# Optimization experiments

Hardware: AMD Instinct MI355X
Metric: run time of the kernel (lower is better)

Reference implementation:

```python
import jax, jax.numpy as jnp
import numpy as np

# config (matches init_kwargs)
B, H, N, D = 2, 8, 2048, 64
ALPHA = 1.0        # < 2 -> power-law kernel branch
D_INT = 4.0        # d_intrinsic
BW = 1.0           # bandwidth
A = 0.5            # dual-sided degree-normalization exponent
R = 1.0            # sphere_radius
MASK_VAL = 10000.0
EPS = 1e-7


def setup_inputs() -> dict:
    key = jax.random.key(0)
    k1, k2, k3, k4 = jax.random.split(key, 4)
    Q = jax.random.normal(k1, (B, H, N, D), dtype=jnp.float32)
    K = jax.random.normal(k2, (B, H, N, D), dtype=jnp.float32)
    V = jax.random.normal(k3, (B, H, N, D), dtype=jnp.float32)
    mask = jax.random.randint(k4, (B, N), 0, 2).astype(jnp.int32)
    return {"Q": Q, "K": K, "V": V, "mask": mask}


def reference(Q, K, V, mask) -> jnp.ndarray:
    # geodesic distance on the sphere: acos(clamp(QK^T)) * radius  [B,H,N,N]
    qk = jnp.einsum('bhnd,bhmd->bhnm', Q, K)
    g_dist = jnp.arccos(jnp.clip(qk, -1.0 + EPS, 1.0 - EPS)) * R
    # key-side padding mask: [B,N] -> [B,1,1,N]
    g_dist = jnp.where(mask[:, None, None, :] == 0, MASK_VAL, g_dist)
    # power-law kernel (alpha < 2 branch)
    attn_score = (1.0 + g_dist / jnp.sqrt(BW)) ** (-D_INT - ALPHA)
    # dual-sided degree normalization (a != 0 branch)
    n_r = jnp.sum(attn_score, axis=-1)   # row degrees [B,H,N]
    n_c = jnp.sum(attn_score, axis=-2)   # col degrees [B,H,N]
    k_tilde = (n_r ** (-A))[..., :, None] * attn_score * (n_c ** (-A))[..., None, :]
    # F.normalize(p=1, dim=3)
    attn = k_tilde / jnp.maximum(jnp.sum(jnp.abs(k_tilde), axis=-1, keepdims=True), 1e-12)
    # dropout p=0.0 -> identity
    return jnp.einsum('bhnm,bhmd->bhnd', attn, V)
```

## Files before the change

### kernel.cpp

```cpp
#include <hip/hip_runtime.h>
#include <hip/hip_bf16.h>
#include <math.h>

#define B_ 2
#define H_ 8
#define N_ 2048
#define D_ 64
#define BH_ 16
#define NT_ (N_/64)
#define LS 72
#define LSW (LS/2)

typedef __attribute__((ext_vector_type(8))) short short8;
typedef __attribute__((ext_vector_type(4))) float float4v;
typedef __attribute__((ext_vector_type(2))) float float2v;

__device__ __forceinline__ float2v splat2(float s){ float2v v; v.x=s; v.y=s; return v; }

__device__ __forceinline__ unsigned packbf2(float a, float b){
  __hip_bfloat162 h = __float22bfloat162_rn(make_float2(a, b));
  return *(unsigned*)&h;
}
__device__ __forceinline__ void split2(float a, float b, unsigned& hi, unsigned& lo){
  hi = packbf2(a, b);
  float ha = __uint_as_float(hi << 16);
  float hb = __uint_as_float(hi & 0xFFFF0000u);
  lo = packbf2(a - ha, b - hb);
}
__device__ __forceinline__ void load_split8(const float* p, short8& hi8, short8& lo8){
  float4v v0 = *(const float4v*)p;
  float4v v1 = *(const float4v*)(p + 4);
  unsigned h0,h1,h2,h3,l0,l1,l2,l3;
  split2(v0.x, v0.y, h0, l0);
  split2(v0.z, v0.w, h1, l1);
  split2(v1.x, v1.y, h2, l2);
  split2(v1.z, v1.w, h3, l3);
  unsigned ph[4] = {h0,h1,h2,h3};
  unsigned pl[4] = {l0,l1,l2,l3};
  hi8 = *(short8*)ph;
  lo8 = *(short8*)pl;
}

__device__ __forceinline__ float2v score2(float2v qk){
  float2v ax;
  ax.x = fminf(fabsf(qk.x), 1.0f - 1e-7f);
  ax.y = fminf(fabsf(qk.y), 1.0f - 1e-7f);
  float2v p = __builtin_elementwise_fma(
                __builtin_elementwise_fma(
                  __builtin_elementwise_fma(splat2(-0.0187293f), ax, splat2(0.0742610f)),
                  ax, splat2(-0.2121144f)),
                ax, splat2(1.5707288f));
  float2v u = __builtin_elementwise_fma(ax, splat2(-1.0f), splat2(1.0f));
  float2v t;
  t.x = __builtin_amdgcn_sqrtf(u.x);
  t.y = __builtin_amdgcn_sqrtf(u.y);
  float2v t2 = t * p;
  float2v gn = __builtin_elementwise_fma(t2, splat2(-1.0f), splat2(3.14159265358979f));
  float2v g;
  g.x = (qk.x >= 0.0f) ? t2.x : gn.x;
  g.y = (qk.y >= 0.0f) ? t2.y : gn.y;
  float2v w1 = g + splat2(1.0f);
  float2v w2 = w1 * w1;
  float2v w4 = w2 * w2;
  float2v w5 = w4 * w1;
  float2v r;
  r.x = __builtin_amdgcn_rcpf(w5.x);
  r.y = __builtin_amdgcn_rcpf(w5.y);
  return r;
}

__device__ __forceinline__ float score_fn_m(float qk, float masked){
  float ax = fminf(fabsf(qk), 1.0f - 1e-7f);
  float t  = __builtin_amdgcn_sqrtf(1.0f - ax);
  float p  = __builtin_fmaf(__builtin_fmaf(__builtin_fmaf(-0.0187293f, ax, 0.0742610f),
                                           ax, -0.2121144f), ax, 1.5707288f);
  float t2 = t * p;
  float g  = (qk >= 0.0f) ? t2 : (3.14159265358979f - t2);
  g = (masked != 0.0f) ? 10000.0f : g;
  float w1 = 1.0f + g;
  float w2 = w1*w1;
  float w4 = w2*w2;
  return __builtin_amdgcn_rcpf(w4*w1);
}

__global__ __launch_bounds__(256) void k0_split(
    const float* __restrict__ Q, const float* __restrict__ K,
    unsigned short* __restrict__ Qh, unsigned short* __restrict__ Ql,
    unsigned short* __restrict__ Kh, unsigned short* __restrict__ Kl)
{
  size_t i = (size_t)blockIdx.x*256 + threadIdx.x;
  const size_t tot = (size_t)BH_*N_*D_/8;
  const float* src; unsigned short *dh, *dl;
  if (i < tot){ src = Q; dh = Qh; dl = Ql; }
  else        { src = K; dh = Kh; dl = Kl; i -= tot; }
  short8 hi, lo;
  load_split8(src + i*8, hi, lo);
  *(short8*)&dh[i*8] = hi;
  *(short8*)&dl[i*8] = lo;
}

template<bool PRE>
__global__ __launch_bounds__(256) void k1_score(
    const float* __restrict__ Qf, const float* __restrict__ Kf,
    const unsigned short* __restrict__ Qh, const unsigned short* __restrict__ Ql,
    const unsigned short* __restrict__ Kh, const unsigned short* __restrict__ Kl,
    float* __restrict__ ncw, unsigned short* __restrict__ S)
{
  __shared__ float red[64*4];
  const int kt = blockIdx.x, bh = blockIdx.y, rz = blockIdx.z;
  const int nz = gridDim.z;
  const int tid = threadIdx.x;
  const int wv = tid>>6, lane = tid&63, quad = lane>>4, l15 = lane&15;

  short8 khi[4][2], klo[4][2];
  if constexpr (PRE){
    #pragma unroll
    for (int s=0;s<4;++s){
      const size_t r = (size_t)(bh*N_ + kt*64 + s*16 + l15)*D_ + quad*8;
      khi[s][0] = *(const short8*)&Kh[r];
      khi[s][1] = *(const short8*)&Kh[r+32];
      klo[s][0] = *(const short8*)&Kl[r];
      klo[s][1] = *(const short8*)&Kl[r+32];
    }
  } else {
    #pragma unroll
    for (int s=0;s<4;++s){
      const float* kp = Kf + (size_t)(bh*N_ + kt*64 + s*16 + l15)*D_ + quad*8;
      load_split8(kp,      khi[s][0], klo[s][0]);
      load_split8(kp + 32, khi[s][1], klo[s][1]);
    }
  }

  float2v cs2[4][2];
  #pragma unroll
  for (int s=0;s<4;++s){ cs2[s][0] = splat2(0.f); cs2[s][1] = splat2(0.f); }

  const int iters = NT_/nz;
  const int rt0 = rz*iters;

  const size_t qoff0 = (size_t)(bh*N_ + rt0*64 + wv*16 + l15)*D_ + quad*8;
  const unsigned lconst = (unsigned)(((quad>>1)<<7) + (l15<<3) + ((quad&1)<<2));
  unsigned short* Sp = S + ((((size_t)(bh*NT_ + kt)*NT_ + rt0)*4 + wv)<<10) + lconst;

  short8 qh0,qh1,ql0,ql1;
  if constexpr (PRE){
    const unsigned short* qp = Qh + qoff0;
    const unsigned short* lp = Ql + qoff0;
    qh0 = *(const short8*)qp;      qh1 = *(const short8*)(qp+32);
    ql0 = *(const short8*)lp;      ql1 = *(const short8*)(lp+32);
  } else {
    const float* qp = Qf + qoff0;
    load_split8(qp,      qh0, ql0);
    load_split8(qp + 32, qh1, ql1);
  }

  for (int rti=0; rti<iters; ++rti){
    short8 nh0,nh1,nl0,nl1;
    const size_t qoffn = qoff0 + (size_t)(rti + ((rti+1<iters) ? 1 : 0))*4096;
    if constexpr (PRE){
      const unsigned short* qp = Qh + qoffn;
      const unsigned short* lp = Ql + qoffn;
      nh0 = *(const short8*)qp;    nh1 = *(const short8*)(qp+32);
      nl0 = *(const short8*)lp;    nl1 = *(const short8*)(lp+32);
    } else {
      const float* qp = Qf + qoffn;
      load_split8(qp,      nh0, nl0);
      load_split8(qp + 32, nh1, nl1);
    }

    #pragma unroll
    for (int s=0;s<4;++s){
      float4v c = {0.f,0.f,0.f,0.f};
      c = __builtin_amdgcn_mfma_f32_16x16x32_bf16(khi[s][0], qh0, c, 0,0,0);
      c = __builtin_amdgcn_mfma_f32_16x16x32_bf16(khi[s][0], ql0, c, 0,0,0);
      c = __builtin_amdgcn_mfma_f32_16x16x32_bf16(klo[s][0], qh0, c, 0,0,0);
      c = __builtin_amdgcn_mfma_f32_16x16x32_bf16(khi[s][1], qh1, c, 0,0,0);
      c = __builtin_amdgcn_mfma_f32_16x16x32_bf16(khi[s][1], ql1, c, 0,0,0);
      c = __builtin_amdgcn_mfma_f32_16x16x32_bf16(klo[s][1], qh1, c, 0,0,0);
      float2v c01; c01.x = c[0]; c01.y = c[1];
      float2v c23; c23.x = c[2]; c23.y = c[3];
      float2v s01 = score2(c01);
      float2v s23 = score2(c23);
      cs2[s][0] += s01;
      cs2[s][1] += s23;
      uint2 pk;
      pk.x = packbf2(s01.x, s01.y);
      pk.y = packbf2(s23.x, s23.y);
      *(uint2*)(Sp + (s<<8)) = pk;
    }
    Sp += 4096;
    qh0=nh0; qh1=nh1; ql0=nl0; ql1=nl1;
  }

  float cs[4][4];
  #pragma unroll
  for (int s=0;s<4;++s){
    cs[s][0]=cs2[s][0].x; cs[s][1]=cs2[s][0].y;
    cs[s][2]=cs2[s][1].x; cs[s][3]=cs2[s][1].y;
  }

  #pragma unroll
  for (int s=0;s<4;++s)
    #pragma unroll
    for (int i=0;i<4;++i){
      float v2 = cs[s][i];
      v2 += __shfl_xor(v2, 1);
      v2 += __shfl_xor(v2, 2);
      v2 += __shfl_xor(v2, 4);
      v2 += __shfl_xor(v2, 8);
      cs[s][i] = v2;
    }
  if (l15 == 0){
    #pragma unroll
    for (int s=0;s<4;++s)
      #pragma unroll
      for (int i=0;i<4;++i)
        red[(s*16 + quad*4 + i)*4 + wv] = cs[s][i];
  }
  __syncthreads();
  if (tid < 64){
    float t = red[tid*4+0] + red[tid*4+1] + red[tid*4+2] + red[tid*4+3];
    atomicAdd(&ncw[bh*N_ + kt*64 + tid], t);
  }
}

__global__ __launch_bounds__(256) void k2_pack(
    const float* __restrict__ V, const float* __restrict__ nc,
    const int* __restrict__ mask, unsigned short* __restrict__ Vw)
{
  __shared__ float T[64*65];
  __shared__ float wrow[64];
  const int mt = blockIdx.x, bh = blockIdx.y;
  const int tid = threadIdx.x;
  const float* Vg = V + (size_t)bh*N_*D_;
  const float* ncg = nc + (size_t)bh*N_;
  unsigned short* Fb = Vw + ((size_t)(bh*NT_ + mt)*10)*512;

  {
    int m = tid >> 2;
    int d0 = (tid & 3) * 16;
    int gm = mt*64 + m;
    float wm = (mask[(bh>>3)*N_ + gm] == 0) ? 0.0f
             : (1.0f / sqrtf(fmaxf(ncg[gm], 1e-30f)));
    if (d0 == 0) wrow[m] = wm;
    #pragma unroll
    for (int j=0;j<4;++j){
      float4v v = *(const float4v*)(Vg + (size_t)gm*D_ + d0 + j*4);
      T[(d0+j*4+0)*65 + m] = v.x*wm;
      T[(d0+j*4+1)*65 + m] = v.y*wm;
      T[(d0+j*4+2)*65 + m] = v.z*wm;
      T[(d0+j*4+3)*65 + m] = v.w*wm;
    }
  }
  __syncthreads();

  for (int idx = tid; idx < 640; idx += 256){
    int f = idx >> 6, lane = idx & 63;
    int quad = lane >> 4, l15 = lane & 15;
    int s2 = f >> 1, cc = f & 1;
    int m0 = cc*32 + quad*8;
    unsigned pk[4];
    if (s2 < 4){
      int d = s2*16 + l15;
      #pragma unroll
      for (int j=0;j<4;++j)
        pk[j] = packbf2(T[d*65 + m0 + 2*j], T[d*65 + m0 + 2*j + 1]);
    } else if (l15 == 0){
      #pragma unroll
      for (int j=0;j<4;++j)
        pk[j] = packbf2(wrow[m0 + 2*j], wrow[m0 + 2*j + 1]);
    } else {
      pk[0]=pk[1]=pk[2]=pk[3]=0u;
    }
    *(short8*)(Fb + ((size_t)f*64 + lane)*8) = *(short8*)pk;
  }
}

__global__ __launch_bounds__(1024) void k3_lds(
    const unsigned short* __restrict__ S, const unsigned short* __restrict__ Vw,
    float* __restrict__ out)
{
  __shared__ unsigned short Vs[2*2*10*512];

  const int rtp = blockIdx.x, bh = blockIdx.y;
  const int tid = threadIdx.x;
  const int wvid = tid >> 6;
  const int g    = wvid >> 3;
  const int slot = wvid & 7;
  const int lane = tid & 63, quad = lane >> 4, l15 = lane & 15;

  const int row = rtp*128 + slot*16 + l15;
  const int rt  = rtp*2 + (slot>>2);

  const size_t sb0 = ((((size_t)bh*NT_ + g*16)*NT_ + rt)*4 + (size_t)(slot&3))*1024
                   + (size_t)quad*128 + (size_t)l15*8;

  float4v acc[4];
  #pragma unroll
  for (int i=0;i<4;++i) acc[i] = (float4v){0.f,0.f,0.f,0.f};
  float4v c5 = {0.f,0.f,0.f,0.f};

  for (int c = tid; c < 1280; c += 1024){
    const int gg = (c >= 640) ? 1 : 0;
    const int rem = c - gg*640;
    const int f = rem >> 6, ln = rem & 63;
    const int kt = gg*16;
    *(short8*)&Vs[(((0*2 + gg)*10 + f) << 9) + ln*8] =
      *(const short8*)&Vw[(((size_t)(bh*NT_ + kt)*10 + f) << 9) + ln*8];
  }
  short8 npf0, npf1;
  npf0 = *(const short8*)&S[sb0];
  npf1 = *(const short8*)&S[sb0 + 512];
  __syncthreads();

  for (int it = 0; it < 16; ++it){
    const int cur = it & 1, nxt = cur ^ 1;
    short8 pf0 = npf0, pf1 = npf1;
    if (it < 15){
      const size_t sb = sb0 + (size_t)(it+1)*131072;
      npf0 = *(const short8*)&S[sb];
      npf1 = *(const short8*)&S[sb + 512];
      for (int c = tid; c < 1280; c += 1024){
        const int gg = (c >= 640) ? 1 : 0;
        const int rem = c - gg*640;
        const int f = rem >> 6, ln = rem & 63;
        const int kt2 = gg*16 + it + 1;
        *(short8*)&Vs[(((nxt*2 + gg)*10 + f) << 9) + ln*8] =
          *(const short8*)&Vw[(((size_t)(bh*NT_ + kt2)*10 + f) << 9) + ln*8];
      }
    }
    const unsigned short* Fl = &Vs[((cur*2 + g)*10) << 9] + (size_t)lane*8;
    short8 va[10];
    #pragma unroll
    for (int f=0; f<10; ++f)
      va[f] = *(const short8*)(Fl + ((size_t)f << 9));

    #pragma unroll
    for (int s2=0;s2<4;++s2){
      acc[s2] = __builtin_amdgcn_mfma_f32_16x16x32_bf16(va[s2*2+0], pf0, acc[s2], 0,0,0);
      acc[s2] = __builtin_amdgcn_mfma_f32_16x16x32_bf16(va[s2*2+1], pf1, acc[s2], 0,0,0);
    }
    c5 = __builtin_amdgcn_mfma_f32_16x16x32_bf16(va[8], pf0, c5, 0,0,0);
    c5 = __builtin_amdgcn_mfma_f32_16x16x32_bf16(va[9], pf1, c5, 0,0,0);

    __syncthreads();
  }

  float* Red = (float*)Vs;
  if (g == 1){
    float* Rr = Red + (size_t)(slot*16 + l15)*68;
    #pragma unroll
    for (int s2=0;s2<4;++s2)
      #pragma unroll
      for (int i=0;i<4;++i)
        Rr[s2*16 + quad*4 + i] = acc[s2][i];
    if (quad == 0) Rr[64] = c5[0];
  }
  __syncthreads();
  if (g == 0){
    const float* Rr = Red + (size_t)(slot*16 + l15)*68;
    #pragma unroll
    for (int s2=0;s2<4;++s2)
      #pragma unroll
      for (int i=0;i<4;++i)
        acc[s2][i] += Rr[s2*16 + quad*4 + i];
    float rs = __shfl(c5[0], l15) + Rr[64];
    float inv = 1.0f / fmaxf(rs, 1e-12f);

    float* Og = out + (size_t)bh*N_*D_ + (size_t)row*D_;
    #pragma unroll
    for (int s2=0;s2<4;++s2)
      #pragma unroll
      for (int i=0;i<4;++i)
        Og[s2*16 + quad*4 + i] = acc[s2][i] * inv;
  }
}

__global__ __launch_bounds__(256) void k1_fallback(
    const float* __restrict__ Q, const float* __restrict__ K,
    const int* __restrict__ mask, float* __restrict__ ncw)
{
  __shared__ float msk[64];
  __shared__ float red[64*4];
  const int kt = blockIdx.x, bh = blockIdx.y;
  const int tid = threadIdx.x;
  const int wv = tid>>6, lane = tid&63, quad = lane>>4, l15 = lane&15;

  const float* Qg = Q + (size_t)bh*N_*D_;
  const float* Kg = K + (size_t)bh*N_*D_;

  short8 khi[4][2], klo[4][2];
  #pragma unroll
  for (int s=0;s<4;++s){
    const float* kp = Kg + (size_t)(kt*64 + s*16 + l15)*D_ + quad*8;
    load_split8(kp,      khi[s][0], klo[s][0]);
    load_split8(kp + 32, khi[s][1], klo[s][1]);
  }
  if (tid < 64)
    msk[tid] = (mask[(bh>>3)*N_ + kt*64 + tid] == 0) ? 1.f : 0.f;
  __syncthreads();

  float cs[4][4];
  #pragma unroll
  for (int s=0;s<4;++s)
    #pragma unroll
    for (int i=0;i<4;++i) cs[s][i] = 0.f;

  for (int rt=0; rt<NT_; ++rt){
    const float* qp = Qg + (size_t)(rt*64 + wv*16 + l15)*D_ + quad*8;
    short8 bhi[2], blo[2];
    load_split8(qp,      bhi[0], blo[0]);
    load_split8(qp + 32, bhi[1], blo[1]);

    #pragma unroll
    for (int s=0;s<4;++s){
      float4v c = {0.f,0.f,0.f,0.f};
      #pragma unroll
      for (int cc=0; cc<2; ++cc){
        c = __builtin_amdgcn_mfma_f32_16x16x32_bf16(khi[s][cc], bhi[cc], c, 0,0,0);
        c = __builtin_amdgcn_mfma_f32_16x16x32_bf16(khi[s][cc], blo[cc], c, 0,0,0);
        c = __builtin_amdgcn_mfma_f32_16x16x32_bf16(klo[s][cc], bhi[cc], c, 0,0,0);
      }
      int kl = s*16 + quad*4;
      cs[s][0] += score_fn_m(c[0], msk[kl+0]);
      cs[s][1] += score_fn_m(c[1], msk[kl+1]);
      cs[s][2] += score_fn_m(c[2], msk[kl+2]);
      cs[s][3] += score_fn_m(c[3], msk[kl+3]);
    }
  }

  #pragma unroll
  for (int s=0;s<4;++s)
    #pragma unroll
    for (int i=0;i<4;++i){
      float v2 = cs[s][i];
      v2 += __shfl_xor(v2, 1);
      v2 += __shfl_xor(v2, 2);
      v2 += __shfl_xor(v2, 4);
      v2 += __shfl_xor(v2, 8);
      cs[s][i] = v2;
    }
  if (l15 == 0){
    #pragma unroll
    for (int s=0;s<4;++s)
      #pragma unroll
      for (int i=0;i<4;++i)
        red[(s*16 + quad*4 + i)*4 + wv] = cs[s][i];
  }
  __syncthreads();
  if (tid < 64){
    float t = red[tid*4+0] + red[tid*4+1] + red[tid*4+2] + red[tid*4+3];
    ncw[bh*N_ + kt*64 + tid] = 1.0f / sqrtf(t);
  }
}

__global__ __launch_bounds__(256) void spop_pass2(
    const float* __restrict__ Q, const float* __restrict__ K,
    const float* __restrict__ V, const int* __restrict__ mask,
    const float* __restrict__ w, float* __restrict__ out)
{
  __shared__ unsigned short Khi[64*LS], Klo[64*LS];
  __shared__ unsigned short Vt[64*LS];
  __shared__ unsigned short Ps[64*LS];
  __shared__ float msk[64], wms[64];

  const int rt = blockIdx.x, bh = blockIdx.y, b = bh>>3;
  const int tid = threadIdx.x;
  const int wv = tid>>6, lane = tid&63, quad = lane>>4, l15 = lane&15;

  const float* Qg = Q + (size_t)bh*N_*D_;
  const float* Kg = K + (size_t)bh*N_*D_;
  const float* Vg = V + (size_t)bh*N_*D_;

  short8 qhi[2], qlo[2];
  {
    const float* qp = Qg + (size_t)(rt*64 + wv*16 + l15)*D_ + quad*8;
    load_split8(qp,      qhi[0], qlo[0]);
    load_split8(qp + 32, qhi[1], qlo[1]);
  }

  float4v acc[4];
  #pragma unroll
  for (int i=0;i<4;++i) acc[i] = (float4v){0.f,0.f,0.f,0.f};
  float rs = 0.f;

  for (int kt=0; kt<NT_; ++kt){
    __syncthreads();
    #pragma unroll
    for (int it=0; it<4; ++it){
      int idx = tid + it*256;
      int r = idx>>4, d4 = (idx&15)<<2;
      const float4v v = *(const float4v*)(Kg + (size_t)(kt*64 + r)*D_ + d4);
      unsigned h0,l0,h1,l1;
      split2(v.x, v.y, h0, l0);
      split2(v.z, v.w, h1, l1);
      unsigned* KhiW = (unsigned*)Khi; unsigned* KloW = (unsigned*)Klo;
      int base = r*LSW + (d4>>1);
      KhiW[base] = h0; KhiW[base+1] = h1;
      KloW[base] = l0; KloW[base+1] = l1;
    }
    #pragma unroll
    for (int it=0; it<2; ++it){
      int u = tid + it*256;
      int kp = u & 31;
      int d4 = (u>>5)<<2;
      const float* vp = Vg + (size_t)(kt*64 + kp*2)*D_ + d4;
      float4v a0 = *(const float4v*)vp;
      float4v a1 = *(const float4v*)(vp + D_);
      unsigned* VtW = (unsigned*)Vt;
      VtW[(d4+0)*LSW + kp] = packbf2(a0.x, a1.x);
      VtW[(d4+1)*LSW + kp] = packbf2(a0.y, a1.y);
      VtW[(d4+2)*LSW + kp] = packbf2(a0.z, a1.z);
      VtW[(d4+3)*LSW + kp] = packbf2(a0.w, a1.w);
    }
    if (tid < 64){
      int gk = kt*64 + tid;
      msk[tid] = (mask[b*N_ + gk] == 0) ? 1.f : 0.f;
      wms[tid] = w[bh*N_ + gk];
    }
    __syncthreads();

    #pragma unroll
    for (int s=0;s<4;++s){
      float4v c = {0.f,0.f,0.f,0.f};
      #pragma unroll
      for (int cc=0; cc<2; ++cc){
        const short8 ahi = *(const short8*)&Khi[(s*16+l15)*LS + cc*32 + quad*8];
        const short8 alo = *(const short8*)&Klo[(s*16+l15)*LS + cc*32 + quad*8];
        c = __builtin_amdgcn_mfma_f32_16x16x32_bf16(ahi, qhi[cc], c, 0,0,0);
        c = __builtin_amdgcn_mfma_f32_16x16x32_bf16(ahi, qlo[cc], c, 0,0,0);
        c = __builtin_amdgcn_mfma_f32_16x16x32_bf16(alo, qhi[cc], c, 0,0,0);
      }
      int kl = s*16 + quad*4;
      float sc0 = score_fn_m(c[0], msk[kl+0]) * wms[kl+0];
      float sc1 = score_fn_m(c[1], msk[kl+1]) * wms[kl+1];
      float sc2 = score_fn_m(c[2], msk[kl+2]) * wms[kl+2];
      float sc3 = score_fn_m(c[3], msk[kl+3]) * wms[kl+3];
      rs += (sc0 + sc1) + (sc2 + sc3);
      unsigned* PsW = (unsigned*)Ps;
      int pb = (wv*16 + l15)*LSW + (kl>>1);
      PsW[pb]   = packbf2(sc0, sc1);
      PsW[pb+1] = packbf2(sc2, sc3);
    }

    short8 pf[2];
    pf[0] = *(const short8*)&Ps[(wv*16+l15)*LS +  0 + quad*8];
    pf[1] = *(const short8*)&Ps[(wv*16+l15)*LS + 32 + quad*8];
    #pragma unroll
    for (int s2=0;s2<4;++s2){
      #pragma unroll
      for (int cc=0; cc<2; ++cc){
        const short8 av = *(const short8*)&Vt[(s2*16+l15)*LS + cc*32 + quad*8];
        acc[s2] = __builtin_amdgcn_mfma_f32_16x16x32_bf16(av, pf[cc], acc[s2], 0,0,0);
      }
    }
  }

  rs += __shfl_xor(rs, 16);
  rs += __shfl_xor(rs, 32);
  float inv = 1.0f / fmaxf(rs, 1e-12f);

  float* Og = out + (size_t)bh*N_*D_ + (size_t)(rt*64 + wv*16 + l15)*D_;
  #pragma unroll
  for (int s2=0;s2<4;++s2)
    #pragma unroll
    for (int i=0;i<4;++i)
      Og[s2*16 + quad*4 + i] = acc[s2][i] * inv;
}

extern "C" void kernel_launch(void* const* d_in, const int* in_sizes, int n_in,
                              void* d_out, int out_size, void* d_ws, size_t ws_size,
                              hipStream_t stream) {
  (void)in_sizes; (void)n_in; (void)out_size;
  const float* Q   = (const float*)d_in[0];
  const float* K   = (const float*)d_in[1];
  const float* V   = (const float*)d_in[2];
  const int*  mask = (const int*)d_in[3];
  float* out = (float*)d_out;

  const size_t nc_bytes = (size_t)BH_*N_*sizeof(float);
  const size_t vw_off   = 131072;
  const size_t vw_bytes = (size_t)BH_*NT_*10*512*2;
  const size_t qk_off   = vw_off + vw_bytes;
  const size_t qk_one   = (size_t)BH_*N_*D_;
  const size_t qk_bytes = 4*qk_one*2;
  const size_t S_bytes  = (size_t)2*BH_*N_*N_;
  const size_t need_A   = qk_off + qk_bytes + S_bytes;
  const size_t need_B   = qk_off + S_bytes;

  if (ws_size >= need_A){
    float* nc = (float*)d_ws;
    unsigned short* Vw = (unsigned short*)((char*)d_ws + vw_off);
    unsigned short* Qh = (unsigned short*)((char*)d_ws + qk_off);
    unsigned short* Ql = Qh + qk_one;
    unsigned short* Kh = Ql + qk_one;
    unsigned short* Kl = Kh + qk_one;
    unsigned short* S  = (unsigned short*)((char*)d_ws + qk_off + qk_bytes);
    hipMemsetAsync(nc, 0, nc_bytes, stream);
    k0_split<<<dim3(2048), 256, 0, stream>>>(Q, K, Qh, Ql, Kh, Kl);
    k1_score<true><<<dim3(NT_, BH_, 4), 256, 0, stream>>>(
        nullptr, nullptr, Qh, Ql, Kh, Kl, nc, S);
    k2_pack<<<dim3(NT_, BH_), 256, 0, stream>>>(V, nc, mask, Vw);
    k3_lds<<<dim3(N_/128, BH_), 1024, 0, stream>>>(S, Vw, out);
  } else if (ws_size >= need_B){
    float* nc = (float*)d_ws;
    unsigned short* Vw = (unsigned short*)((char*)d_ws + vw_off);
    unsigned short* S  = (unsigned short*)((char*)d_ws + qk_off);
    hipMemsetAsync(nc, 0, nc_bytes, stream);
    k1_score<false><<<dim3(NT_, BH_, 4), 256, 0, stream>>>(
        Q, K, nullptr, nullptr, nullptr, nullptr, nc, S);
    k2_pack<<<dim3(NT_, BH_), 256, 0, stream>>>(V, nc, mask, Vw);
    k3_lds<<<dim3(N_/128, BH_), 1024, 0, stream>>>(S, Vw, out);
  } else {
    float* w = (float*)d_ws;
    k1_fallback<<<dim3(NT_, BH_), 256, 0, stream>>>(Q, K, mask, w);
    spop_pass2<<<dim3(NT_, BH_), 256, 0, stream>>>(Q, K, V, mask, w, out);
  }
}
```

Baseline: 171.4 us.

## Give each score wave its own key tile and defer V staging stores past MFMAs

The score kernel now assigns each wave a distinct 16-key slice and loops over all query row tiles with one MFMA chain per iteration. This drops the shared-memory reduction and barrier in favour of per-wave atomics, and adds a launch-bounds occupancy hint. The PV kernel loads the next V tile into registers before the MFMAs and writes it to LDS afterwards, so global latency overlaps compute. The trade-off is four times more Q reloads per block, more atomics, and no Q prefetch across iterations.

```diff
diff --git a/kernel.cpp b/kernel.cpp
--- a/kernel.cpp
+++ b/kernel.cpp
@@ -100,127 +100,87 @@
 }
 
 template<bool PRE>
-__global__ __launch_bounds__(256) void k1_score(
+__global__ __launch_bounds__(256, 8) void k1_score(
     const float* __restrict__ Qf, const float* __restrict__ Kf,
     const unsigned short* __restrict__ Qh, const unsigned short* __restrict__ Ql,
     const unsigned short* __restrict__ Kh, const unsigned short* __restrict__ Kl,
     float* __restrict__ ncw, unsigned short* __restrict__ S)
 {
-  __shared__ float red[64*4];
   const int kt = blockIdx.x, bh = blockIdx.y, rz = blockIdx.z;
   const int nz = gridDim.z;
   const int tid = threadIdx.x;
   const int wv = tid>>6, lane = tid&63, quad = lane>>4, l15 = lane&15;
 
-  short8 khi[4][2], klo[4][2];
-  if constexpr (PRE){
-    #pragma unroll
-    for (int s=0;s<4;++s){
-      const size_t r = (size_t)(bh*N_ + kt*64 + s*16 + l15)*D_ + quad*8;
-      khi[s][0] = *(const short8*)&Kh[r];
-      khi[s][1] = *(const short8*)&Kh[r+32];
-      klo[s][0] = *(const short8*)&Kl[r];
-      klo[s][1] = *(const short8*)&Kl[r+32];
-    }
-  } else {
-    #pragma unroll
-    for (int s=0;s<4;++s){
-      const float* kp = Kf + (size_t)(bh*N_ + kt*64 + s*16 + l15)*D_ + quad*8;
-      load_split8(kp,      khi[s][0], klo[s][0]);
-      load_split8(kp + 32, khi[s][1], klo[s][1]);
-    }
-  }
-
-  float2v cs2[4][2];
-  #pragma unroll
-  for (int s=0;s<4;++s){ cs2[s][0] = splat2(0.f); cs2[s][1] = splat2(0.f); }
-
-  const int iters = NT_/nz;
-  const int rt0 = rz*iters;
-
-  const size_t qoff0 = (size_t)(bh*N_ + rt0*64 + wv*16 + l15)*D_ + quad*8;
-  const unsigned lconst = (unsigned)(((quad>>1)<<7) + (l15<<3) + ((quad&1)<<2));
-  unsigned short* Sp = S + ((((size_t)(bh*NT_ + kt)*NT_ + rt0)*4 + wv)<<10) + lconst;
-
-  short8 qh0,qh1,ql0,ql1;
-  if constexpr (PRE){
-    const unsigned short* qp = Qh + qoff0;
-    const unsigned short* lp = Ql + qoff0;
-    qh0 = *(const short8*)qp;      qh1 = *(const short8*)(qp+32);
-    ql0 = *(const short8*)lp;      ql1 = *(const short8*)(lp+32);
-  } else {
-    const float* qp = Qf + qoff0;
-    load_split8(qp,      qh0, ql0);
-    load_split8(qp + 32, qh1, ql1);
-  }
-
-  for (int rti=0; rti<iters; ++rti){
-    short8 nh0,nh1,nl0,nl1;
-    const size_t qoffn = qoff0 + (size_t)(rti + ((rti+1<iters) ? 1 : 0))*4096;
+  short8 khi[2], klo[2];
+  {
+    const size_t r = (size_t)(bh*N_ + kt*64 + wv*16 + l15)*D_ + quad*8;
     if constexpr (PRE){
-      const unsigned short* qp = Qh + qoffn;
-      const unsigned short* lp = Ql + qoffn;
-      nh0 = *(const short8*)qp;    nh1 = *(const short8*)(qp+32);
-      nl0 = *(const short8*)lp;    nl1 = *(const short8*)(lp+32);
+      khi[0] = *(const short8*)&Kh[r];
+      khi[1] = *(const short8*)&Kh[r+32];
+      klo[0] = *(const short8*)&Kl[r];
+      klo[1] = *(const short8*)&Kl[r+32];
     } else {
-      const float* qp = Qf + qoffn;
-      load_split8(qp,      nh0, nl0);
-      load_split8(qp + 32, nh1, nl1);
-    }
-
-    #pragma unroll
-    for (int s=0;s<4;++s){
-      float4v c = {0.f,0.f,0.f,0.f};
-      c = __builtin_amdgcn_mfma_f32_16x16x32_bf16(khi[s][0], qh0, c, 0,0,0);
-      c = __builtin_amdgcn_mfma_f32_16x16x32_bf16(khi[s][0], ql0, c, 0,0,0);
-      c = __builtin_amdgcn_mfma_f32_16x16x32_bf16(klo[s][0], qh0, c, 0,0,0);
-      c = __builtin_amdgcn_mfma_f32_16x16x32_bf16(khi[s][1], qh1, c, 0,0,0);
-      c = __builtin_amdgcn_mfma_f32_16x16x32_bf16(khi[s][1], ql1, c, 0,0,0);
-      c = __builtin_amdgcn_mfma_f32_16x16x32_bf16(klo[s][1], qh1, c, 0,0,0);
-      float2v c01; c01.x = c[0]; c01.y = c[1];
-      float2v c23; c23.x = c[2]; c23.y = c[3];
-      float2v s01 = score2(c01);
-      float2v s23 = score2(c23);
-      cs2[s][0] += s01;
-      cs2[s][1] += s23;
-      uint2 pk;
-      pk.x = packbf2(s01.x, s01.y);
-      pk.y = packbf2(s23.x, s23.y);
-      *(uint2*)(Sp + (s<<8)) = pk;
-    }
-    Sp += 4096;
-    qh0=nh0; qh1=nh1; ql0=nl0; ql1=nl1;
-  }
-
-  float cs[4][4];
-  #pragma unroll
-  for (int s=0;s<4;++s){
-    cs[s][0]=cs2[s][0].x; cs[s][1]=cs2[s][0].y;
-    cs[s][2]=cs2[s][1].x; cs[s][3]=cs2[s][1].y;
-  }
-
-  #pragma unroll
-  for (int s=0;s<4;++s)
-    #pragma unroll
-    for (int i=0;i<4;++i){
-      float v2 = cs[s][i];
-      v2 += __shfl_xor(v2, 1);
-      v2 += __shfl_xor(v2, 2);
-      v2 += __shfl_xor(v2, 4);
-      v2 += __shfl_xor(v2, 8);
-      cs[s][i] = v2;
-    }
+      load_split8(Kf + r,      khi[0], klo[0]);
+      load_split8(Kf + r + 32, khi[1], klo[1]);
+    }
+  }
+
+  float2v cs01 = splat2(0.f), cs23 = splat2(0.f);
+
+  const int iters = (N_/16)/nz;
+  const int row0  = rz*(N_/nz);
+
+  size_t qoff = (size_t)(bh*N_ + row0 + l15)*D_ + quad*8;
+  const unsigned lconst = (unsigned)((wv<<8) + ((quad>>1)<<7) + (l15<<3) + ((quad&1)<<2));
+  unsigned short* Sp = S + (((size_t)(bh*NT_ + kt)*128 + (unsigned)(row0>>4))<<10) + lconst;
+
+  for (int j=0; j<iters; ++j){
+    short8 qh0,qh1,ql0,ql1;
+    if constexpr (PRE){
+      qh0 = *(const short8*)&Qh[qoff];  qh1 = *(const short8*)&Qh[qoff+32];
+      ql0 = *(const short8*)&Ql[qoff];  ql1 = *(const short8*)&Ql[qoff+32];
+    } else {
+      load_split8(Qf + qoff,      qh0, ql0);
+      load_split8(Qf + qoff + 32, qh1, ql1);
+    }
+
+    float4v c = {0.f,0.f,0.f,0.f};
+    c = __builtin_amdgcn_mfma_f32_16x16x32_bf16(khi[0], qh0, c, 0,0,0);
+    c = __builtin_amdgcn_mfma_f32_16x16x32_bf16(khi[0], ql0, c, 0,0,0);
+    c = __builtin_amdgcn_mfma_f32_16x16x32_bf16(klo[0], qh0, c, 0,0,0);
+    c = __builtin_amdgcn_mfma_f32_16x16x32_bf16(khi[1], qh1, c, 0,0,0);
+    c = __builtin_amdgcn_mfma_f32_16x16x32_bf16(khi[1], ql1, c, 0,0,0);
+    c = __builtin_amdgcn_mfma_f32_16x16x32_bf16(klo[1], qh1, c, 0,0,0);
+
+    float2v c01; c01.x = c[0]; c01.y = c[1];
+    float2v c23; c23.x = c[2]; c23.y = c[3];
+    float2v s01 = score2(c01);
+    float2v s23 = score2(c23);
+    cs01 += s01;
+    cs23 += s23;
+    uint2 pk;
+    pk.x = packbf2(s01.x, s01.y);
+    pk.y = packbf2(s23.x, s23.y);
+    *(uint2*)Sp = pk;
+
+    Sp += 1024;
+    qoff += (size_t)16*D_;
+  }
+
+  float cs[4] = {cs01.x, cs01.y, cs23.x, cs23.y};
+  #pragma unroll
+  for (int i=0;i<4;++i){
+    float v2 = cs[i];
+    v2 += __shfl_xor(v2, 1);
+    v2 += __shfl_xor(v2, 2);
+    v2 += __shfl_xor(v2, 4);
+    v2 += __shfl_xor(v2, 8);
+    cs[i] = v2;
+  }
   if (l15 == 0){
     #pragma unroll
-    for (int s=0;s<4;++s)
-      #pragma unroll
-      for (int i=0;i<4;++i)
-        red[(s*16 + quad*4 + i)*4 + wv] = cs[s][i];
-  }
-  __syncthreads();
-  if (tid < 64){
-    float t = red[tid*4+0] + red[tid*4+1] + red[tid*4+2] + red[tid*4+3];
-    atomicAdd(&ncw[bh*N_ + kt*64 + tid], t);
+    for (int i=0;i<4;++i)
+      atomicAdd(&ncw[bh*N_ + kt*64 + wv*16 + quad*4 + i], cs[i]);
   }
 }
 
@@ -295,40 +255,44 @@
   const size_t sb0 = ((((size_t)bh*NT_ + g*16)*NT_ + rt)*4 + (size_t)(slot&3))*1024
                    + (size_t)quad*128 + (size_t)l15*8;
 
+  const int gg0 = (tid >= 640) ? 1 : 0;
+  const int rem0 = tid - gg0*640;
+  const int f0 = rem0 >> 6, ln0 = rem0 & 63;
+  const bool has1 = (tid < 256);
+  const int rem1 = tid + 384;
+  const int f1 = rem1 >> 6, ln1 = rem1 & 63;
+  const size_t vwbh = (size_t)bh*NT_;
+
   float4v acc[4];
   #pragma unroll
   for (int i=0;i<4;++i) acc[i] = (float4v){0.f,0.f,0.f,0.f};
   float4v c5 = {0.f,0.f,0.f,0.f};
 
-  for (int c = tid; c < 1280; c += 1024){
-    const int gg = (c >= 640) ? 1 : 0;
-    const int rem = c - gg*640;
-    const int f = rem >> 6, ln = rem & 63;
-    const int kt = gg*16;
-    *(short8*)&Vs[(((0*2 + gg)*10 + f) << 9) + ln*8] =
-      *(const short8*)&Vw[(((size_t)(bh*NT_ + kt)*10 + f) << 9) + ln*8];
-  }
-  short8 npf0, npf1;
-  npf0 = *(const short8*)&S[sb0];
-  npf1 = *(const short8*)&S[sb0 + 512];
+  {
+    short8 a = *(const short8*)&Vw[(((vwbh + gg0*16)*10 + f0) << 9) + ln0*8];
+    *(short8*)&Vs[((gg0*10 + f0) << 9) + ln0*8] = a;
+    if (has1){
+      short8 b = *(const short8*)&Vw[(((vwbh + 16)*10 + f1) << 9) + ln1*8];
+      *(short8*)&Vs[((1*10 + f1) << 9) + ln1*8] = b;
+    }
+  }
+  short8 npf0 = *(const short8*)&S[sb0];
+  short8 npf1 = *(const short8*)&S[sb0 + 512];
   __syncthreads();
 
   for (int it = 0; it < 16; ++it){
     const int cur = it & 1, nxt = cur ^ 1;
     short8 pf0 = npf0, pf1 = npf1;
+    short8 vwa, vwb;
     if (it < 15){
+      vwa = *(const short8*)&Vw[(((vwbh + (size_t)(gg0*16 + it + 1))*10 + f0) << 9) + ln0*8];
+      if (has1)
+        vwb = *(const short8*)&Vw[(((vwbh + (size_t)(16 + it + 1))*10 + f1) << 9) + ln1*8];
       const size_t sb = sb0 + (size_t)(it+1)*131072;
       npf0 = *(const short8*)&S[sb];
       npf1 = *(const short8*)&S[sb + 512];
-      for (int c = tid; c < 1280; c += 1024){
-        const int gg = (c >= 640) ? 1 : 0;
-        const int rem = c - gg*640;
-        const int f = rem >> 6, ln = rem & 63;
-        const int kt2 = gg*16 + it + 1;
-        *(short8*)&Vs[(((nxt*2 + gg)*10 + f) << 9) + ln*8] =
-          *(const short8*)&Vw[(((size_t)(bh*NT_ + kt2)*10 + f) << 9) + ln*8];
-      }
-    }
+    }
+
     const unsigned short* Fl = &Vs[((cur*2 + g)*10) << 9] + (size_t)lane*8;
     short8 va[10];
     #pragma unroll
@@ -343,6 +307,11 @@
     c5 = __builtin_amdgcn_mfma_f32_16x16x32_bf16(va[8], pf0, c5, 0,0,0);
     c5 = __builtin_amdgcn_mfma_f32_16x16x32_bf16(va[9], pf1, c5, 0,0,0);
 
+    if (it < 15){
+      *(short8*)&Vs[(((nxt*2 + gg0)*10 + f0) << 9) + ln0*8] = vwa;
+      if (has1)
+        *(short8*)&Vs[(((nxt*2 + 1)*10 + f1) << 9) + ln1*8] = vwb;
+    }
     __syncthreads();
   }
 
```

Measured after the change: 231.1 us. 34.9% more time.

## Replace LDS-staged V tiles with direct global loads in final matmul kernel

Applied to the files above, without the earlier changes.

The final S·V kernel stops staging packed V fragments through double-buffered shared memory with per-iteration barriers. Each wave now loads its V fragments straight from global memory (relying on cache), and S fragments are prefetched two tiles ahead with two register sets. Blocks shrink from 1024 to 512 threads covering 64 rows instead of 128, which doubles the grid. V reuse across waves now depends on L1/L2 hits rather than explicit shared-memory sharing.

```diff
diff --git a/kernel.cpp b/kernel.cpp
--- a/kernel.cpp
+++ b/kernel.cpp
@@ -276,77 +276,79 @@
   }
 }
 
-__global__ __launch_bounds__(1024) void k3_lds(
+__global__ __launch_bounds__(512) void k3_direct(
     const unsigned short* __restrict__ S, const unsigned short* __restrict__ Vw,
     float* __restrict__ out)
 {
-  __shared__ unsigned short Vs[2*2*10*512];
-
-  const int rtp = blockIdx.x, bh = blockIdx.y;
+  __shared__ float Red[64*68];
+
+  const int rt = blockIdx.x, bh = blockIdx.y;
   const int tid = threadIdx.x;
   const int wvid = tid >> 6;
-  const int g    = wvid >> 3;
-  const int slot = wvid & 7;
+  const int g    = wvid >> 2;
+  const int slot = wvid & 3;
   const int lane = tid & 63, quad = lane >> 4, l15 = lane & 15;
-
-  const int row = rtp*128 + slot*16 + l15;
-  const int rt  = rtp*2 + (slot>>2);
-
-  const size_t sb0 = ((((size_t)bh*NT_ + g*16)*NT_ + rt)*4 + (size_t)(slot&3))*1024
+  const int row = rt*64 + slot*16 + l15;
+
+  const size_t sb0 = ((((size_t)bh*NT_ + g*16)*NT_ + rt)*4 + (size_t)slot)*1024
                    + (size_t)quad*128 + (size_t)l15*8;
+  const unsigned short* Vb = Vw + ((size_t)(bh*NT_ + g*16)*10)*512 + (size_t)lane*8;
 
   float4v acc[4];
   #pragma unroll
   for (int i=0;i<4;++i) acc[i] = (float4v){0.f,0.f,0.f,0.f};
   float4v c5 = {0.f,0.f,0.f,0.f};
 
-  for (int c = tid; c < 1280; c += 1024){
-    const int gg = (c >= 640) ? 1 : 0;
-    const int rem = c - gg*640;
-    const int f = rem >> 6, ln = rem & 63;
-    const int kt = gg*16;
-    *(short8*)&Vs[(((0*2 + gg)*10 + f) << 9) + ln*8] =
-      *(const short8*)&Vw[(((size_t)(bh*NT_ + kt)*10 + f) << 9) + ln*8];
-  }
-  short8 npf0, npf1;
-  npf0 = *(const short8*)&S[sb0];
-  npf1 = *(const short8*)&S[sb0 + 512];
-  __syncthreads();
-
-  for (int it = 0; it < 16; ++it){
-    const int cur = it & 1, nxt = cur ^ 1;
-    short8 pf0 = npf0, pf1 = npf1;
-    if (it < 15){
-      const size_t sb = sb0 + (size_t)(it+1)*131072;
-      npf0 = *(const short8*)&S[sb];
-      npf1 = *(const short8*)&S[sb + 512];
-      for (int c = tid; c < 1280; c += 1024){
-        const int gg = (c >= 640) ? 1 : 0;
-        const int rem = c - gg*640;
-        const int f = rem >> 6, ln = rem & 63;
-        const int kt2 = gg*16 + it + 1;
-        *(short8*)&Vs[(((nxt*2 + gg)*10 + f) << 9) + ln*8] =
-          *(const short8*)&Vw[(((size_t)(bh*NT_ + kt2)*10 + f) << 9) + ln*8];
+  short8 sA0 = *(const short8*)&S[sb0];
+  short8 sA1 = *(const short8*)&S[sb0 + 512];
+  short8 sB0 = *(const short8*)&S[sb0 + 131072];
+  short8 sB1 = *(const short8*)&S[sb0 + 131072 + 512];
+
+  #pragma unroll 1
+  for (int k2 = 0; k2 < 8; ++k2){
+    const int ktA = k2*2, ktB = k2*2 + 1;
+    {
+      const unsigned short* Vp = Vb + (size_t)ktA*5120;
+      short8 va[10];
+      #pragma unroll
+      for (int f=0; f<10; ++f)
+        va[f] = *(const short8*)(Vp + (size_t)f*512);
+      short8 p0 = sA0, p1 = sA1;
+      if (ktA + 2 < 16){
+        const size_t sb = sb0 + (size_t)(ktA+2)*131072;
+        sA0 = *(const short8*)&S[sb];
+        sA1 = *(const short8*)&S[sb + 512];
       }
-    }
-    const unsigned short* Fl = &Vs[((cur*2 + g)*10) << 9] + (size_t)lane*8;
-    short8 va[10];
-    #pragma unroll
-    for (int f=0; f<10; ++f)
-      va[f] = *(const short8*)(Fl + ((size_t)f << 9));
-
-    #pragma unroll
-    for (int s2=0;s2<4;++s2){
-      acc[s2] = __builtin_amdgcn_mfma_f32_16x16x32_bf16(va[s2*2+0], pf0, acc[s2], 0,0,0);
-      acc[s2] = __builtin_amdgcn_mfma_f32_16x16x32_bf16(va[s2*2+1], pf1, acc[s2], 0,0,0);
-    }
-    c5 = __builtin_amdgcn_mfma_f32_16x16x32_bf16(va[8], pf0, c5, 0,0,0);
-    c5 = __builtin_amdgcn_mfma_f32_16x16x32_bf16(va[9], pf1, c5, 0,0,0);
-
-    __syncthreads();
-  }
-
-  float* Red = (float*)Vs;
+      #pragma unroll
+      for (int s2=0;s2<4;++s2){
+        acc[s2] = __builtin_amdgcn_mfma_f32_16x16x32_bf16(va[s2*2+0], p0, acc[s2], 0,0,0);
+        acc[s2] = __builtin_amdgcn_mfma_f32_16x16x32_bf16(va[s2*2+1], p1, acc[s2], 0,0,0);
+      }
+      c5 = __builtin_amdgcn_mfma_f32_16x16x32_bf16(va[8], p0, c5, 0,0,0);
+      c5 = __builtin_amdgcn_mfma_f32_16x16x32_bf16(va[9], p1, c5, 0,0,0);
+    }
+    {
+      const unsigned short* Vp = Vb + (size_t)ktB*5120;
+      short8 va[10];
+      #pragma unroll
+      for (int f=0; f<10; ++f)
+        va[f] = *(const short8*)(Vp + (size_t)f*512);
+      short8 p0 = sB0, p1 = sB1;
+      if (ktB + 2 < 16){
+        const size_t sb = sb0 + (size_t)(ktB+2)*131072;
+        sB0 = *(const short8*)&S[sb];
+        sB1 = *(const short8*)&S[sb + 512];
+      }
+      #pragma unroll
+      for (int s2=0;s2<4;++s2){
+        acc[s2] = __builtin_amdgcn_mfma_f32_16x16x32_bf16(va[s2*2+0], p0, acc[s2], 0,0,0);
+        acc[s2] = __builtin_amdgcn_mfma_f32_16x16x32_bf16(va[s2*2+1], p1, acc[s2], 0,0,0);
+      }
+      c5 = __builtin_amdgcn_mfma_f32_16x16x32_bf16(va[8], p0, c5, 0,0,0);
+      c5 = __builtin_amdgcn_mfma_f32_16x16x32_bf16(va[9], p1, c5, 0,0,0);
+    }
+  }
+
   if (g == 1){
     float* Rr = Red + (size_t)(slot*16 + l15)*68;
     #pragma unroll
@@ -601,7 +603,7 @@
     k1_score<true><<<dim3(NT_, BH_, 4), 256, 0, stream>>>(
         nullptr, nullptr, Qh, Ql, Kh, Kl, nc, S);
     k2_pack<<<dim3(NT_, BH_), 256, 0, stream>>>(V, nc, mask, Vw);
-    k3_lds<<<dim3(N_/128, BH_), 1024, 0, stream>>>(S, Vw, out);
+    k3_direct<<<dim3(NT_, BH_), 512, 0, stream>>>(S, Vw, out);
   } else if (ws_size >= need_B){
     float* nc = (float*)d_ws;
     unsigned short* Vw = (unsigned short*)((char*)d_ws + vw_off);
@@ -610,7 +612,7 @@
     k1_score<false><<<dim3(NT_, BH_, 4), 256, 0, stream>>>(
         Q, K, nullptr, nullptr, nullptr, nullptr, nc, S);
     k2_pack<<<dim3(NT_, BH_), 256, 0, stream>>>(V, nc, mask, Vw);
-    k3_lds<<<dim3(N_/128, BH_), 1024, 0, stream>>>(S, Vw, out);
+    k3_direct<<<dim3(NT_, BH_), 512, 0, stream>>>(S, Vw, out);
   } else {
     float* w = (float*)d_ws;
     k1_fallback<<<dim3(NT_, BH_), 256, 0, stream>>>(Q, K, mask, w);
```

Measured after the change: 171.8 us. No clear change (+0.2%).

## Remap block ids so each XCD owns whole heads; register-stage V prefetch

Applied to the files above, without the earlier changes.

Launches k1, k2 and k3 as flat 1D grids and decodes block ids so that all blocks touching the same (batch, head) land on the same XCD (id & 7). This is meant to keep each head's K/Q/S/V traffic inside one XCD's L2 instead of spreading it across all eight. In k3 the next V tile is now loaded into registers before the MFMA work and written to LDS after it, rather than copied to LDS right away. The copy loop is also replaced by precomputed per-thread indices, which lets the global load latency overlap with compute at the cost of extra registers.

```diff
diff --git a/kernel.cpp b/kernel.cpp
--- a/kernel.cpp
+++ b/kernel.cpp
@@ -107,8 +107,14 @@
     float* __restrict__ ncw, unsigned short* __restrict__ S)
 {
   __shared__ float red[64*4];
-  const int kt = blockIdx.x, bh = blockIdx.y, rz = blockIdx.z;
-  const int nz = gridDim.z;
+  const int id = blockIdx.x;
+  const int xcd = id & 7;
+  const int r0 = id >> 3;
+  const int kt = r0 & 31;
+  const int grp = r0 >> 5;
+  const int flat = grp*8 + xcd;
+  const int bh = flat & 15;
+  const int rz = flat >> 4;
   const int tid = threadIdx.x;
   const int wv = tid>>6, lane = tid&63, quad = lane>>4, l15 = lane&15;
 
@@ -135,7 +141,7 @@
   #pragma unroll
   for (int s=0;s<4;++s){ cs2[s][0] = splat2(0.f); cs2[s][1] = splat2(0.f); }
 
-  const int iters = NT_/nz;
+  const int iters = NT_/4;
   const int rt0 = rz*iters;
 
   const size_t qoff0 = (size_t)(bh*N_ + rt0*64 + wv*16 + l15)*D_ + quad*8;
@@ -230,7 +236,11 @@
 {
   __shared__ float T[64*65];
   __shared__ float wrow[64];
-  const int mt = blockIdx.x, bh = blockIdx.y;
+  const int id = blockIdx.x;
+  const int xcd = id & 7;
+  const int r0 = id >> 3;
+  const int bh = (r0 & 1)*8 + xcd;
+  const int mt = r0 >> 1;
   const int tid = threadIdx.x;
   const float* Vg = V + (size_t)bh*N_*D_;
   const float* ncg = nc + (size_t)bh*N_;
@@ -276,13 +286,18 @@
   }
 }
 
-__global__ __launch_bounds__(1024) void k3_lds(
+__global__ __launch_bounds__(1024) void k3_stage(
     const unsigned short* __restrict__ S, const unsigned short* __restrict__ Vw,
     float* __restrict__ out)
 {
   __shared__ unsigned short Vs[2*2*10*512];
 
-  const int rtp = blockIdx.x, bh = blockIdx.y;
+  const int id = blockIdx.x;
+  const int xcd = id & 7;
+  const int r0 = id >> 3;
+  const int bh  = (r0 & 1)*8 + xcd;
+  const int rtp = r0 >> 1;
+
   const int tid = threadIdx.x;
   const int wvid = tid >> 6;
   const int g    = wvid >> 3;
@@ -295,40 +310,44 @@
   const size_t sb0 = ((((size_t)bh*NT_ + g*16)*NT_ + rt)*4 + (size_t)(slot&3))*1024
                    + (size_t)quad*128 + (size_t)l15*8;
 
+  const int gg0 = (tid >= 640) ? 1 : 0;
+  const int rem0 = tid - gg0*640;
+  const int f0 = rem0 >> 6, ln0 = rem0 & 63;
+  const bool has1 = (tid < 256);
+  const int rem1 = tid + 384;
+  const int f1 = rem1 >> 6, ln1 = rem1 & 63;
+  const size_t vwbh = (size_t)bh*NT_;
+
   float4v acc[4];
   #pragma unroll
   for (int i=0;i<4;++i) acc[i] = (float4v){0.f,0.f,0.f,0.f};
   float4v c5 = {0.f,0.f,0.f,0.f};
 
-  for (int c = tid; c < 1280; c += 1024){
-    const int gg = (c >= 640) ? 1 : 0;
-    const int rem = c - gg*640;
-    const int f = rem >> 6, ln = rem & 63;
-    const int kt = gg*16;
-    *(short8*)&Vs[(((0*2 + gg)*10 + f) << 9) + ln*8] =
-      *(const short8*)&Vw[(((size_t)(bh*NT_ + kt)*10 + f) << 9) + ln*8];
-  }
-  short8 npf0, npf1;
-  npf0 = *(const short8*)&S[sb0];
-  npf1 = *(const short8*)&S[sb0 + 512];
+  {
+    short8 a = *(const short8*)&Vw[(((vwbh + gg0*16)*10 + f0) << 9) + ln0*8];
+    *(short8*)&Vs[((gg0*10 + f0) << 9) + ln0*8] = a;
+    if (has1){
+      short8 b = *(const short8*)&Vw[(((vwbh + 16)*10 + f1) << 9) + ln1*8];
+      *(short8*)&Vs[((1*10 + f1) << 9) + ln1*8] = b;
+    }
+  }
+  short8 npf0 = *(const short8*)&S[sb0];
+  short8 npf1 = *(const short8*)&S[sb0 + 512];
   __syncthreads();
 
   for (int it = 0; it < 16; ++it){
     const int cur = it & 1, nxt = cur ^ 1;
     short8 pf0 = npf0, pf1 = npf1;
+    short8 vwa, vwb;
     if (it < 15){
+      vwa = *(const short8*)&Vw[(((vwbh + (size_t)(gg0*16 + it + 1))*10 + f0) << 9) + ln0*8];
+      if (has1)
+        vwb = *(const short8*)&Vw[(((vwbh + (size_t)(16 + it + 1))*10 + f1) << 9) + ln1*8];
       const size_t sb = sb0 + (size_t)(it+1)*131072;
       npf0 = *(const short8*)&S[sb];
       npf1 = *(const short8*)&S[sb + 512];
-      for (int c = tid; c < 1280; c += 1024){
-        const int gg = (c >= 640) ? 1 : 0;
-        const int rem = c - gg*640;
-        const int f = rem >> 6, ln = rem & 63;
-        const int kt2 = gg*16 + it + 1;
-        *(short8*)&Vs[(((nxt*2 + gg)*10 + f) << 9) + ln*8] =
-          *(const short8*)&Vw[(((size_t)(bh*NT_ + kt2)*10 + f) << 9) + ln*8];
-      }
-    }
+    }
+
     const unsigned short* Fl = &Vs[((cur*2 + g)*10) << 9] + (size_t)lane*8;
     short8 va[10];
     #pragma unroll
@@ -343,6 +362,11 @@
     c5 = __builtin_amdgcn_mfma_f32_16x16x32_bf16(va[8], pf0, c5, 0,0,0);
     c5 = __builtin_amdgcn_mfma_f32_16x16x32_bf16(va[9], pf1, c5, 0,0,0);
 
+    if (it < 15){
+      *(short8*)&Vs[(((nxt*2 + gg0)*10 + f0) << 9) + ln0*8] = vwa;
+      if (has1)
+        *(short8*)&Vs[(((nxt*2 + 1)*10 + f1) << 9) + ln1*8] = vwb;
+    }
     __syncthreads();
   }
 
@@ -598,19 +622,19 @@
     unsigned short* S  = (unsigned short*)((char*)d_ws + qk_off + qk_bytes);
     hipMemsetAsync(nc, 0, nc_bytes, stream);
     k0_split<<<dim3(2048), 256, 0, stream>>>(Q, K, Qh, Ql, Kh, Kl);
-    k1_score<true><<<dim3(NT_, BH_, 4), 256, 0, stream>>>(
+    k1_score<true><<<dim3(2048), 256, 0, stream>>>(
         nullptr, nullptr, Qh, Ql, Kh, Kl, nc, S);
-    k2_pack<<<dim3(NT_, BH_), 256, 0, stream>>>(V, nc, mask, Vw);
-    k3_lds<<<dim3(N_/128, BH_), 1024, 0, stream>>>(S, Vw, out);
+    k2_pack<<<dim3(512), 256, 0, stream>>>(V, nc, mask, Vw);
+    k3_stage<<<dim3(256), 1024, 0, stream>>>(S, Vw, out);
   } else if (ws_size >= need_B){
     float* nc = (float*)d_ws;
     unsigned short* Vw = (unsigned short*)((char*)d_ws + vw_off);
     unsigned short* S  = (unsigned short*)((char*)d_ws + qk_off);
     hipMemsetAsync(nc, 0, nc_bytes, stream);
-    k1_score<false><<<dim3(NT_, BH_, 4), 256, 0, stream>>>(
+    k1_score<false><<<dim3(2048), 256, 0, stream>>>(
         Q, K, nullptr, nullptr, nullptr, nullptr, nc, S);
-    k2_pack<<<dim3(NT_, BH_), 256, 0, stream>>>(V, nc, mask, Vw);
-    k3_lds<<<dim3(N_/128, BH_), 1024, 0, stream>>>(S, Vw, out);
+    k2_pack<<<dim3(512), 256, 0, stream>>>(V, nc, mask, Vw);
+    k3_stage<<<dim3(256), 1024, 0, stream>>>(S, Vw, out);
   } else {
     float* w = (float*)d_ws;
     k1_fallback<<<dim3(NT_, BH_), 256, 0, stream>>>(Q, K, mask, w);
```

After: 164.3 us. -4.1%, faster.
